# Performance work log

Measured on AMD Instinct MI355X. Metric: run time of the kernel, lower is better.

The kernel has to match this reference:

```python
import jax, jax.numpy as jnp
import numpy as np

N_NODES = 10000

def setup_inputs() -> dict:
    key = jax.random.key(0)
    k1, k2, k3, k4 = jax.random.split(key, 4)
    N, E, D, H = N_NODES, 320000, 128, 256
    x = jax.random.normal(k1, (N, D), dtype=jnp.float32)
    edge_index = jax.random.randint(k2, (2, E), 0, N, dtype=jnp.int32)
    edge_weight = jax.random.uniform(k3, (E,), dtype=jnp.float32)
    W_enc = jax.random.normal(k4, (D, H), dtype=jnp.float32) * 0.05
    return {"x": x, "edge_index": edge_index, "edge_weight": edge_weight, "W_enc": W_enc}

def _random_walk_matrix(edge_index, edge_weight, num_nodes):
    # sparse COO -> dense (coalescing duplicate edges by summation, as torch does)
    adj = jnp.zeros((num_nodes, num_nodes), dtype=edge_weight.dtype)
    adj = adj.at[edge_index[0], edge_index[1]].add(edge_weight)
    # faithful to original: adj / (adj.sum(dim=1) + eps), broadcasting over last axis
    return adj / (adj.sum(axis=1) + 1e-20)

def reference(x, edge_index, edge_weight, W_enc):
    num_nodes = x.shape[0]
    # augmentors are identity: (x1, ei1, ew1) == (x2, ei2, ew2) == inputs
    rw1 = _random_walk_matrix(edge_index, edge_weight, num_nodes)
    rw2 = rw1
    # encoder modeled as a single linear map (opaque GNN submodule stub)
    z = x @ W_enc
    z1 = z
    z2 = z
    return (z, z1, z2, rw1, rw2)
```

## Files before the change

### kernel.cpp

```cpp
#include <hip/hip_runtime.h>
#include <hip/hip_bf16.h>

#define N_NODES 10000
#define N_EDGES 320000
#define DIM_D   128
#define DIM_H   256

#define Z_ELEMS   (N_NODES * DIM_H)
#define RW_ELEMS  ((size_t)N_NODES * N_NODES)
#define OFF_Z1    ((size_t)Z_ELEMS)
#define OFF_Z2    ((size_t)2 * Z_ELEMS)
#define OFF_RW1   ((size_t)3 * Z_ELEMS)
#define OFF_RW2   (OFF_RW1 + RW_ELEMS)

#define WS_ROWSUM 0
#define WS_CNT    40960
#define WS_CURSOR 81920
#define WS_ROWPTR 122880
#define WS_COL    163840
#define WS_VAL    1443840

#define GEMM_RB 157
#define GEMM_CB 4
#define GEMM_TOTAL (GEMM_RB * GEMM_CB)

typedef float f32x4 __attribute__((ext_vector_type(4)));

__device__ inline void nt_store4(float* p, float4 v) {
    f32x4 t = {v.x, v.y, v.z, v.w};
    __builtin_nontemporal_store(t, (f32x4*)p);
}

__global__ void count_kernel(const int* __restrict__ ei,
                             const float* __restrict__ ew,
                             float* __restrict__ rowsum,
                             int* __restrict__ cnt, int E) {
    int e = blockIdx.x * blockDim.x + threadIdx.x;
    if (e >= E) return;
    int s = ei[e];
    atomicAdd(&rowsum[s], ew[e]);
    atomicAdd(&cnt[s], 1);
}

__global__ __launch_bounds__(1024) void scan_kernel(const int* __restrict__ cnt,
                                                    int* __restrict__ rowptr) {
    __shared__ int part[1024];
    int t = threadIdx.x;
    int base = t * 10;
    int local[10];
    int s = 0;
    for (int i = 0; i < 10; ++i) {
        int c = (base + i < N_NODES) ? cnt[base + i] : 0;
        local[i] = s;
        s += c;
    }
    part[t] = s;
    __syncthreads();
    for (int off = 1; off < 1024; off <<= 1) {
        int v = part[t];
        int add = (t >= off) ? part[t - off] : 0;
        __syncthreads();
        part[t] = v + add;
        __syncthreads();
    }
    int pre = (t > 0) ? part[t - 1] : 0;
    for (int i = 0; i < 10; ++i) {
        int r = base + i;
        if (r < N_NODES) rowptr[r] = pre + local[i];
    }
    if (t == 1023) rowptr[N_NODES] = part[1023];
}

__global__ void csr_fill_kernel(const int* __restrict__ ei,
                                const float* __restrict__ ew,
                                const float* __restrict__ rowsum,
                                const int* __restrict__ rowptr,
                                int* __restrict__ cursor,
                                int* __restrict__ col,
                                float* __restrict__ val, int E) {
    int e = blockIdx.x * blockDim.x + threadIdx.x;
    if (e >= E) return;
    int s = ei[e];
    int d = ei[E + e];
    int p = rowptr[s] + atomicAdd(&cursor[s], 1);
    col[p] = d;
    val[p] = ew[e] / (rowsum[d] + 1e-20f);
}

__global__ __launch_bounds__(256) void fused_kernel(
        const int* __restrict__ rowptr,
        const int* __restrict__ col,
        const float* __restrict__ val,
        float* __restrict__ rw1,
        float* __restrict__ rw2,
        const float* __restrict__ x,
        const float* __restrict__ W,
        float* __restrict__ out) {
    __shared__ float smem[N_NODES];

    if (blockIdx.x >= GEMM_TOTAL) {
        int r = blockIdx.x - GEMM_TOTAL;
        float4* row4 = reinterpret_cast<float4*>(smem);
        const float4 z4 = make_float4(0.f, 0.f, 0.f, 0.f);

        for (int i = threadIdx.x; i < N_NODES / 4; i += 256) row4[i] = z4;
        __syncthreads();

        int beg = rowptr[r], end = rowptr[r + 1];
        for (int e = beg + threadIdx.x; e < end; e += 256)
            atomicAdd(&smem[col[e]], val[e]);
        __syncthreads();

        float* o1 = rw1 + (size_t)r * N_NODES;
        float* o2 = rw2 + (size_t)r * N_NODES;
        for (int i = threadIdx.x; i < N_NODES / 4; i += 256) {
            float4 v = row4[i];
            nt_store4(o1 + 4 * i, v);
            nt_store4(o2 + 4 * i, v);
        }
        return;
    }

    float* xs = smem;
    float* wsm = smem + 64 * 33;

    int rb = blockIdx.x >> 2;
    int cb = blockIdx.x & 3;
    int r_base = rb * 64;
    int c_base = cb * 64;

    int t  = threadIdx.x;
    int tr = t >> 4;
    int tc = t & 15;

    float acc[4][4];
#pragma unroll
    for (int i = 0; i < 4; ++i)
#pragma unroll
        for (int j = 0; j < 4; ++j) acc[i][j] = 0.f;

    for (int k0 = 0; k0 < DIM_D; k0 += 32) {
#pragma unroll
        for (int q = t; q < 512; q += 256) {
            int row = q >> 3;
            int c4  = q & 7;
            int grow = r_base + row;
            float4 f = (grow < N_NODES)
                ? *reinterpret_cast<const float4*>(x + (size_t)grow * DIM_D + k0 + c4 * 4)
                : make_float4(0.f, 0.f, 0.f, 0.f);
            float* dst = xs + row * 33 + c4 * 4;
            dst[0] = f.x; dst[1] = f.y; dst[2] = f.z; dst[3] = f.w;
        }
#pragma unroll
        for (int q = t; q < 512; q += 256) {
            int kk = q >> 4;
            int c4 = q & 15;
            float4 f = *reinterpret_cast<const float4*>(
                W + (size_t)(k0 + kk) * DIM_H + c_base + c4 * 4);
            *reinterpret_cast<float4*>(wsm + kk * 64 + c4 * 4) = f;
        }
        __syncthreads();

        for (int kk = 0; kk < 32; ++kk) {
            float4 w4 = *reinterpret_cast<const float4*>(wsm + kk * 64 + tc * 4);
#pragma unroll
            for (int i = 0; i < 4; ++i) {
                float a = xs[(tr * 4 + i) * 33 + kk];
                acc[i][0] += a * w4.x;
                acc[i][1] += a * w4.y;
                acc[i][2] += a * w4.z;
                acc[i][3] += a * w4.w;
            }
        }
        __syncthreads();
    }

#pragma unroll
    for (int i = 0; i < 4; ++i) {
        int row = r_base + tr * 4 + i;
        if (row >= N_NODES) continue;
        float4 v = make_float4(acc[i][0], acc[i][1], acc[i][2], acc[i][3]);
        size_t o = (size_t)row * DIM_H + c_base + tc * 4;
        nt_store4(out + o, v);
        nt_store4(out + OFF_Z1 + o, v);
        nt_store4(out + OFF_Z2 + o, v);
    }
}

extern "C" void kernel_launch(void* const* d_in, const int* in_sizes, int n_in,
                              void* d_out, int out_size, void* d_ws, size_t ws_size,
                              hipStream_t stream) {
    const float* x      = (const float*)d_in[0];
    const int*   ei     = (const int*)d_in[1];
    const float* ew     = (const float*)d_in[2];
    const float* W_enc  = (const float*)d_in[3];
    float* out = (float*)d_out;

    char* ws = (char*)d_ws;
    float* rowsum = (float*)(ws + WS_ROWSUM);
    int*   cnt    = (int*)(ws + WS_CNT);
    int*   cursor = (int*)(ws + WS_CURSOR);
    int*   rowptr = (int*)(ws + WS_ROWPTR);
    int*   col    = (int*)(ws + WS_COL);
    float* val    = (float*)(ws + WS_VAL);

    hipMemsetAsync(ws, 0, WS_ROWPTR, stream);

    count_kernel<<<(N_EDGES + 255) / 256, 256, 0, stream>>>(ei, ew, rowsum, cnt, N_EDGES);
    scan_kernel<<<1, 1024, 0, stream>>>(cnt, rowptr);
    csr_fill_kernel<<<(N_EDGES + 255) / 256, 256, 0, stream>>>(
        ei, ew, rowsum, rowptr, cursor, col, val, N_EDGES);

    fused_kernel<<<GEMM_TOTAL + N_NODES, 256, 0, stream>>>(
        rowptr, col, val, out + OFF_RW1, out + OFF_RW2, x, W_enc, out);
}
```

Measured before the change: 241.5 us.

## Split rw1/rw2 row writes into separate blocks, widen blocks to 512 threads

Each dense random-walk row is now built by two separate blocks, one per output copy, and each writes a single destination. The previous version had one block write both copies. Blocks grow to 512 threads, and the GEMM tile grows to 128 rows so the block count stays consistent. Nontemporal stores are replaced with plain float4 stores. The goal is more parallelism and memory-level concurrency for the 800MB store stream, at the cost of doing the shared-memory scatter twice per row.

Result: faster. 234.9 us (-2.7%).

```diff
diff --git a/kernel.cpp b/kernel.cpp
--- a/kernel.cpp
+++ b/kernel.cpp
@@ -20,16 +20,9 @@
 #define WS_COL    163840
 #define WS_VAL    1443840
 
-#define GEMM_RB 157
+#define GEMM_RB 79
 #define GEMM_CB 4
 #define GEMM_TOTAL (GEMM_RB * GEMM_CB)
-
-typedef float f32x4 __attribute__((ext_vector_type(4)));
-
-__device__ inline void nt_store4(float* p, float4 v) {
-    f32x4 t = {v.x, v.y, v.z, v.w};
-    __builtin_nontemporal_store(t, (f32x4*)p);
-}
 
 __global__ void count_kernel(const int* __restrict__ ei,
                              const float* __restrict__ ew,
@@ -87,7 +80,7 @@
     val[p] = ew[e] / (rowsum[d] + 1e-20f);
 }
 
-__global__ __launch_bounds__(256) void fused_kernel(
+__global__ __launch_bounds__(512) void fused_kernel(
         const int* __restrict__ rowptr,
         const int* __restrict__ col,
         const float* __restrict__ val,
@@ -99,34 +92,33 @@
     __shared__ float smem[N_NODES];
 
     if (blockIdx.x >= GEMM_TOTAL) {
-        int r = blockIdx.x - GEMM_TOTAL;
+        int b = blockIdx.x - GEMM_TOTAL;
+        int r = (b >= N_NODES) ? b - N_NODES : b;
+        float* dst_base = (b >= N_NODES) ? rw2 : rw1;
+
         float4* row4 = reinterpret_cast<float4*>(smem);
         const float4 z4 = make_float4(0.f, 0.f, 0.f, 0.f);
 
-        for (int i = threadIdx.x; i < N_NODES / 4; i += 256) row4[i] = z4;
+        for (int i = threadIdx.x; i < N_NODES / 4; i += 512) row4[i] = z4;
         __syncthreads();
 
         int beg = rowptr[r], end = rowptr[r + 1];
-        for (int e = beg + threadIdx.x; e < end; e += 256)
+        for (int e = beg + threadIdx.x; e < end; e += 512)
             atomicAdd(&smem[col[e]], val[e]);
         __syncthreads();
 
-        float* o1 = rw1 + (size_t)r * N_NODES;
-        float* o2 = rw2 + (size_t)r * N_NODES;
-        for (int i = threadIdx.x; i < N_NODES / 4; i += 256) {
-            float4 v = row4[i];
-            nt_store4(o1 + 4 * i, v);
-            nt_store4(o2 + 4 * i, v);
-        }
+        float4* o = reinterpret_cast<float4*>(dst_base + (size_t)r * N_NODES);
+        for (int i = threadIdx.x; i < N_NODES / 4; i += 512)
+            o[i] = row4[i];
         return;
     }
 
     float* xs = smem;
-    float* wsm = smem + 64 * 33;
+    float* wsm = smem + 128 * 33;
 
     int rb = blockIdx.x >> 2;
     int cb = blockIdx.x & 3;
-    int r_base = rb * 64;
+    int r_base = rb * 128;
     int c_base = cb * 64;
 
     int t  = threadIdx.x;
@@ -141,7 +133,7 @@
 
     for (int k0 = 0; k0 < DIM_D; k0 += 32) {
 #pragma unroll
-        for (int q = t; q < 512; q += 256) {
+        for (int q = t; q < 1024; q += 512) {
             int row = q >> 3;
             int c4  = q & 7;
             int grow = r_base + row;
@@ -151,10 +143,9 @@
             float* dst = xs + row * 33 + c4 * 4;
             dst[0] = f.x; dst[1] = f.y; dst[2] = f.z; dst[3] = f.w;
         }
-#pragma unroll
-        for (int q = t; q < 512; q += 256) {
-            int kk = q >> 4;
-            int c4 = q & 15;
+        {
+            int kk = t >> 4;
+            int c4 = t & 15;
             float4 f = *reinterpret_cast<const float4*>(
                 W + (size_t)(k0 + kk) * DIM_H + c_base + c4 * 4);
             *reinterpret_cast<float4*>(wsm + kk * 64 + c4 * 4) = f;
@@ -181,9 +172,9 @@
         if (row >= N_NODES) continue;
         float4 v = make_float4(acc[i][0], acc[i][1], acc[i][2], acc[i][3]);
         size_t o = (size_t)row * DIM_H + c_base + tc * 4;
-        nt_store4(out + o, v);
-        nt_store4(out + OFF_Z1 + o, v);
-        nt_store4(out + OFF_Z2 + o, v);
+        *reinterpret_cast<float4*>(out + o)          = v;
+        *reinterpret_cast<float4*>(out + OFF_Z1 + o) = v;
+        *reinterpret_cast<float4*>(out + OFF_Z2 + o) = v;
     }
 }
 
@@ -211,6 +202,6 @@
     csr_fill_kernel<<<(N_EDGES + 255) / 256, 256, 0, stream>>>(
         ei, ew, rowsum, rowptr, cursor, col, val, N_EDGES);
 
-    fused_kernel<<<GEMM_TOTAL + N_NODES, 256, 0, stream>>>(
+    fused_kernel<<<GEMM_TOTAL + 2 * N_NODES, 512, 0, stream>>>(
         rowptr, col, val, out + OFF_RW1, out + OFF_RW2, x, W_enc, out);
 }
```
